# Optimization experiments

Hardware: AMD Instinct MI355X
Metric: run time of the kernel (lower is better)

## Reference

```python
import jax, jax.numpy as jnp
import numpy as np

A = 15                    # num_anchor_per_point
H = W = 34                # hardcoded feature map size in the torch module
STRIDE = 16               # heat_map_a
ANCHOR_W = jnp.array([45.3, 32.0, 22.6, 90.5, 64.0, 45.3, 181.0, 128.0, 90.5, 271.5, 192.0, 135.8, 362.0, 256.0, 181.0], dtype=jnp.float32)
ANCHOR_H = jnp.array([22.6, 32.0, 45.3, 45.3, 64.0, 90.5, 90.5, 128.0, 181.0, 135.8, 192.0, 271.5, 181.0, 256.0, 362.0], dtype=jnp.float32)
THRESH_OBJ = 0.2
MIN_H = 6.0
MIN_W = 6.0
MAX_CAND = 5000
TOP_N = 300
OVERLAP = 0.7


def _generate_anchors():
    xmins = -0.5 * (ANCHOR_W - 1.0)
    xmaxs = 0.5 * (ANCHOR_W - 1.0)
    ymins = -0.5 * (ANCHOR_H - 1.0)
    ymaxs = 0.5 * (ANCHOR_H - 1.0)
    return jnp.stack([xmins, ymins, xmaxs, ymaxs], axis=1)  # [A,4]


def _bbox_transform_inv(boxes, deltas):
    widths = boxes[:, 2] - boxes[:, 0] + 1.0
    heights = boxes[:, 3] - boxes[:, 1] + 1.0
    ctr_x = boxes[:, 0] + 0.5 * (widths - 1.0)
    ctr_y = boxes[:, 1] + 0.5 * (heights - 1.0)
    pred_ctr_x = deltas[:, 0] * widths + ctr_x
    pred_ctr_y = deltas[:, 1] * heights + ctr_y
    pred_w = jnp.exp(deltas[:, 2]) * widths
    pred_h = jnp.exp(deltas[:, 3]) * heights
    return jnp.stack([
        pred_ctr_x - 0.5 * (pred_w - 1.0),
        pred_ctr_y - 0.5 * (pred_h - 1.0),
        pred_ctr_x + 0.5 * (pred_w - 1.0),
        pred_ctr_y + 0.5 * (pred_h - 1.0),
    ], axis=1)


def _nms_keep(boxes, valid, thresh):
    # greedy NMS on score-descending boxes; +1 pixel convention matches module
    x1, y1, x2, y2 = boxes[:, 0], boxes[:, 1], boxes[:, 2], boxes[:, 3]
    areas = (x2 - x1 + 1.0) * (y2 - y1 + 1.0)
    iw = jnp.clip(jnp.minimum(x2[:, None], x2[None, :]) - jnp.maximum(x1[:, None], x1[None, :]) + 1.0, 0.0)
    ih = jnp.clip(jnp.minimum(y2[:, None], y2[None, :]) - jnp.maximum(y1[:, None], y1[None, :]) + 1.0, 0.0)
    inter = iw * ih
    iou = inter / (areas[:, None] + areas[None, :] - inter)  # [M,M]
    M = boxes.shape[0]
    idx = jnp.arange(M)

    def body(i, suppressed):
        alive = jnp.logical_not(suppressed[i])
        return suppressed | (alive & (iou[i] > thresh) & (idx > i))

    suppressed = jax.lax.fori_loop(0, M, body, jnp.logical_not(valid))
    return jnp.logical_not(suppressed) & valid


def _forward(rpn_cls_prob_reshape, rpn_bbox_pred, im_info, bbox_mean, bbox_std):
    origin_height = im_info[0].astype(jnp.float32)
    origin_width = im_info[1].astype(jnp.float32)

    # shifts (replicates torch meshgrid indexing='ij' and (y,x,y,x) column order)
    shift_x = jnp.arange(W, dtype=jnp.float32) * STRIDE
    shift_y = jnp.arange(H, dtype=jnp.float32) * STRIDE
    sx, sy = jnp.meshgrid(shift_x, shift_y, indexing='ij')  # [W,H]
    shifts = jnp.stack([sy.ravel(), sx.ravel(), sy.ravel(), sx.ravel()], axis=1)  # [W*H,4]
    anchors = (_generate_anchors()[None, :, :] + shifts[:, None, :]).reshape(-1, 4)  # [W*H*A,4]

    # deltas: [1,4A,34,34] -> (A,4,34,34) -> (34,34,A,4) -> (-1,4)
    deltas = rpn_bbox_pred.reshape(A, 4, H, W).transpose(2, 3, 0, 1).reshape(-1, 4)
    deltas = deltas * bbox_std + bbox_mean
    proposals = _bbox_transform_inv(anchors, deltas)

    # clip to image (refine_out_of_map_bbox=True)
    xs = jnp.clip(proposals[:, 0::2], 0.0, origin_width - 1.0)
    ys = jnp.clip(proposals[:, 1::2], 0.0, origin_height - 1.0)
    proposals = jnp.stack([xs[:, 0], ys[:, 0], xs[:, 1], ys[:, 1]], axis=1)

    # scores: [1,2A,34,34] -> (2,A,HW) -> (HW,A,2) -> (-1,2)
    scores = rpn_cls_prob_reshape.reshape(2, A, -1).transpose(2, 1, 0).reshape(-1, 2)

    # filter (HEIGHT_AND_WIDTH) via masking (jit-friendly, same selected set)
    ws = proposals[:, 2] - proposals[:, 0] + 1.0
    hs = proposals[:, 3] - proposals[:, 1] + 1.0
    keep = (scores[:, 1] > THRESH_OBJ) & (ws >= MIN_W) & (hs >= MIN_H)

    masked_score = jnp.where(keep, scores[:, 1], -1.0)
    top_vals, top_idx = jax.lax.top_k(masked_score, MAX_CAND)  # sorted descending
    cand = proposals[top_idx]
    valid = keep[top_idx]

    kept = _nms_keep(cand, valid, OVERLAP)

    # emit first TOP_N kept boxes in score order, zero-padded, with batch-id col 0
    rank = jnp.cumsum(kept.astype(jnp.int32)) - 1
    dest = jnp.where(kept & (rank < TOP_N), rank, TOP_N)
    out = jnp.zeros((TOP_N + 1, 5), dtype=cand.dtype)
    out = out.at[dest, 1:].set(cand)
    return out[:TOP_N]


def setup_inputs() -> dict:
    key = jax.random.key(0)
    k1, k2 = jax.random.split(key)
    rpn_cls_prob_reshape = jax.random.uniform(k1, (1, 2 * A, H, W), dtype=jnp.float32)
    rpn_bbox_pred = jax.random.normal(k2, (1, 4 * A, H, W), dtype=jnp.float32)
    im_info = jnp.array([544, 544], dtype=jnp.int32)
    bbox_mean = jnp.array([0.0, 0.0, 0.0, 0.0], dtype=jnp.float32)
    bbox_std = jnp.array([0.1, 0.1, 0.2, 0.2], dtype=jnp.float32)
    return {"rpn_cls_prob_reshape": rpn_cls_prob_reshape, "rpn_bbox_pred": rpn_bbox_pred,
            "im_info": im_info, "bbox_mean": bbox_mean, "bbox_std": bbox_std}


def reference(rpn_cls_prob_reshape, rpn_bbox_pred, im_info, bbox_mean, bbox_std):
    return _forward(rpn_cls_prob_reshape, rpn_bbox_pred, im_info, bbox_mean, bbox_std)
```

## Files before the change

### kernel.cpp

```cpp
#include <hip/hip_runtime.h>

#define NA 15
#define GH 34
#define GW 34
#define SP (GH*GW)
#define NB (SP*NA)
#define MAXC 5000
#define TOPN 300
#define NW 80
#define THRESH_OBJ 0.2f
#define NMS_T 0.7f
#define SH 12
#define BLO 0x3E4CCu
#define NBUCK 5120

typedef unsigned long long u64;
typedef unsigned int u32;

__constant__ float c_aw[NA] = {45.3f,32.0f,22.6f,90.5f,64.0f,45.3f,181.0f,128.0f,90.5f,271.5f,192.0f,135.8f,362.0f,256.0f,181.0f};
__constant__ float c_ah[NA] = {22.6f,32.0f,45.3f,45.3f,64.0f,90.5f,90.5f,128.0f,181.0f,135.8f,192.0f,271.5f,181.0f,256.0f,362.0f};

__global__ __launch_bounds__(256) void k_decode(
    const float* __restrict__ cls, const float* __restrict__ pred,
    const int* __restrict__ iminfo, const float* __restrict__ mean,
    const float* __restrict__ stdv, float* __restrict__ boxes,
    u32* __restrict__ sbits, int* __restrict__ hist) {
#pragma clang fp contract(off)
  int r = blockIdx.x * 256 + threadIdx.x;
  if (r >= NB) return;
  int n = r % NA;
  int p = r / NA;
  int w = p % GW;
  int h = p / GW;

  float score = cls[(NA + n) * SP + p];

  float d0 = pred[(n*4+0)*SP + p] * stdv[0] + mean[0];
  float d1 = pred[(n*4+1)*SP + p] * stdv[1] + mean[1];
  float d2 = pred[(n*4+2)*SP + p] * stdv[2] + mean[2];
  float d3 = pred[(n*4+3)*SP + p] * stdv[3] + mean[3];

  float aw = c_aw[n], ah = c_ah[n];
  float sx = (float)(w * 16);
  float sy = (float)(h * 16);
  float xmin = -0.5f * (aw - 1.0f) + sx;
  float ymin = -0.5f * (ah - 1.0f) + sy;
  float xmax =  0.5f * (aw - 1.0f) + sx;
  float ymax =  0.5f * (ah - 1.0f) + sy;

  float widths  = xmax - xmin + 1.0f;
  float heights = ymax - ymin + 1.0f;
  float ctrx = xmin + 0.5f * (widths - 1.0f);
  float ctry = ymin + 0.5f * (heights - 1.0f);

  float pcx = d0 * widths + ctrx;
  float pcy = d1 * heights + ctry;
  float pw = expf(d2) * widths;
  float ph = expf(d3) * heights;

  float x1 = pcx - 0.5f * (pw - 1.0f);
  float y1 = pcy - 0.5f * (ph - 1.0f);
  float x2 = pcx + 0.5f * (pw - 1.0f);
  float y2 = pcy + 0.5f * (ph - 1.0f);

  float ow = (float)iminfo[1] - 1.0f;
  float oh = (float)iminfo[0] - 1.0f;
  x1 = fminf(fmaxf(x1, 0.0f), ow);
  x2 = fminf(fmaxf(x2, 0.0f), ow);
  y1 = fminf(fmaxf(y1, 0.0f), oh);
  y2 = fminf(fmaxf(y2, 0.0f), oh);

  float ws = x2 - x1 + 1.0f;
  float hs = y2 - y1 + 1.0f;
  bool keep = (score > THRESH_OBJ) && (ws >= 6.0f) && (hs >= 6.0f);

  boxes[r*4+0] = x1;
  boxes[r*4+1] = y1;
  boxes[r*4+2] = x2;
  boxes[r*4+3] = y2;

  u32 bits = keep ? __float_as_uint(score) : 0u;
  sbits[r] = bits;
  if (bits) {
    int b = min((int)((bits >> SH) - BLO), NBUCK - 1);
    atomicAdd(&hist[b], 1);
  }
}

__global__ __launch_bounds__(1024) void k_scan(const int* __restrict__ hist,
    int* __restrict__ base, int* __restrict__ cnt) {
  __shared__ int sh[NBUCK];
  __shared__ int ch[1024];
  int tid = threadIdx.x;
  for (int j = tid; j < NBUCK; j += 1024) sh[j] = hist[j];
  __syncthreads();
  int c0 = sh[tid*5+0], c1 = sh[tid*5+1], c2 = sh[tid*5+2], c3 = sh[tid*5+3], c4 = sh[tid*5+4];
  ch[tid] = c0 + c1 + c2 + c3 + c4;
  __syncthreads();
  for (int off = 1; off < 1024; off <<= 1) {
    int v = ch[tid];
    int u = (tid + off < 1024) ? ch[tid + off] : 0;
    __syncthreads();
    ch[tid] = v + u;
    __syncthreads();
  }
  int S = (tid + 1 < 1024) ? ch[tid + 1] : 0;
  int b4 = S;
  int b3 = b4 + c4;
  int b2 = b3 + c3;
  int b1 = b2 + c2;
  int b0 = b1 + c1;
  base[tid*5+0] = b0; base[tid*5+1] = b1; base[tid*5+2] = b2;
  base[tid*5+3] = b3; base[tid*5+4] = b4;
  if (tid == 0) *cnt = ch[0];
}

__global__ __launch_bounds__(256) void k_place(const u32* __restrict__ sbits,
    const int* __restrict__ base, int* __restrict__ fill, u64* __restrict__ blist) {
  int i = blockIdx.x * 256 + threadIdx.x;
  if (i >= NB) return;
  u32 bits = sbits[i];
  if (!bits) return;
  int b = min((int)((bits >> SH) - BLO), NBUCK - 1);
  int pos = base[b] + atomicAdd(&fill[b], 1);
  blist[pos] = ((u64)bits << 32) | (u64)(0xFFFFFFFFu - (u32)i);
}

__global__ __launch_bounds__(256) void k_final(const u32* __restrict__ sbits,
    const int* __restrict__ hist, const int* __restrict__ base,
    const u64* __restrict__ blist, const float* __restrict__ boxes,
    float* __restrict__ sboxes) {
  int i = blockIdx.x * 256 + threadIdx.x;
  if (i >= NB) return;
  u32 bits = sbits[i];
  if (!bits) return;
  int b = min((int)((bits >> SH) - BLO), NBUCK - 1);
  u64 key = ((u64)bits << 32) | (u64)(0xFFFFFFFFu - (u32)i);
  int s = base[b], n = hist[b];
  int r = s;
  for (int p = s; p < s + n; ++p) r += (blist[p] > key) ? 1 : 0;
  if (r < MAXC) ((float4*)sboxes)[r] = ((const float4*)boxes)[i];
}

__global__ __launch_bounds__(64) void k_iou(const float* __restrict__ sboxes,
    const int* __restrict__ cnt, u64* __restrict__ mask) {
#pragma clang fp contract(off)
  int N = min(*cnt, MAXC);
  int bi = blockIdx.x, bj = blockIdx.y;
  int t = threadIdx.x;
  int i = bi * 64 + t;
  if (bj < bi) {
    if (i < N) mask[(size_t)i * NW + bj] = 0ULL;
    return;
  }
  if (bi * 64 >= N) return;
  __shared__ float4 jb[64];
  int j0 = bj * 64;
  if (j0 + t < N) jb[t] = ((const float4*)sboxes)[j0 + t];
  __syncthreads();
  if (i >= N) return;
  float4 a = ((const float4*)sboxes)[i];
  float areaA = (a.z - a.x + 1.0f) * (a.w - a.y + 1.0f);
  u64 word = 0;
  int jmax = min(64, N - j0);
  for (int jj = 0; jj < jmax; ++jj) {
    int j = j0 + jj;
    if (j <= i) continue;
    float4 b = jb[jj];
    float iw = fminf(a.z, b.z) - fmaxf(a.x, b.x) + 1.0f;
    float ih = fminf(a.w, b.w) - fmaxf(a.y, b.y) + 1.0f;
    iw = fmaxf(iw, 0.0f);
    ih = fmaxf(ih, 0.0f);
    float inter = iw * ih;
    float areaB = (b.z - b.x + 1.0f) * (b.w - b.y + 1.0f);
    float iou = inter / (areaA + areaB - inter);
    if (iou > NMS_T) word |= (1ULL << jj);
  }
  mask[(size_t)i * NW + bj] = word;
}

__device__ __forceinline__ u64 rl64(u64 v, int l) {
  unsigned lo = __builtin_amdgcn_readlane((unsigned)(v & 0xffffffffULL), l);
  unsigned hi = __builtin_amdgcn_readlane((unsigned)(v >> 32), l);
  return ((u64)hi << 32) | (u64)lo;
}

__global__ __launch_bounds__(64) void k_nms(const float* __restrict__ sboxes,
    const u64* __restrict__ mask, const int* __restrict__ cnt,
    float* __restrict__ out) {
  const int t = threadIdx.x;
  const int N = min(*cnt, MAXC);
  const int NBLK = (N + 63) >> 6;
  u64 r0 = 0ULL, r1 = 0ULL;
  __shared__ int klist[TOPN];
  int kept = 0;

  u64 colA = 0ULL, colB = 0ULL;
  if (NBLK > 0) colA = mask[(size_t)t * NW + 0];

  for (int b = 0; b < NBLK; ++b) {
    u64 cc = (b & 1) ? colB : colA;
    if (b + 1 < NBLK) {
      u64 nx = mask[(size_t)((b + 1) * 64 + t) * NW + (b + 1)];
      if (b & 1) colA = nx; else colB = nx;
    }
    int base = b * 64;
    int nv = N - base; if (nv > 64) nv = 64;
    u64 valid = (nv >= 64) ? ~0ULL : ((1ULL << nv) - 1ULL);
    u64 w = (b < 64) ? rl64(r0, b) : rl64(r1, b - 64);
    u64 avail = ~w & valid;
    u64 kmask = 0ULL;
    while (avail) {
      int d = __builtin_amdgcn_readfirstlane((int)__builtin_ctzll(avail));
      if (t == 0) klist[kept] = base + d;
      ++kept;
      kmask |= (1ULL << d);
      u64 sup = rl64(cc, d);
      avail &= ~(sup | (1ULL << d));
      if (kept >= TOPN) break;
    }
    if (kept >= TOPN) break;
    while (kmask) {
      u64 km = kmask;
      int n = __popcll(km); if (n > 8) n = 8;
#define NEXTD(dK) int dK = km ? (int)__builtin_ctzll(km) : 0; km &= (km - 1ULL);
      NEXTD(d0) NEXTD(d1) NEXTD(d2) NEXTD(d3) NEXTD(d4) NEXTD(d5) NEXTD(d6) NEXTD(d7)
#undef NEXTD
      kmask = km;
      u64 lo0=0,lo1=0,lo2=0,lo3=0,lo4=0,lo5=0,lo6=0,lo7=0;
      u64 hi0=0,hi1=0,hi2=0,hi3=0,hi4=0,hi5=0,hi6=0,hi7=0;
      int hw = 64 + (t & 15);
#define LOADK(K, dK) if (n > K) { const u64* rp = mask + (size_t)(base + dK) * NW; \
        lo##K = rp[t]; hi##K = rp[hw]; }
      LOADK(0, d0) LOADK(1, d1) LOADK(2, d2) LOADK(3, d3)
      LOADK(4, d4) LOADK(5, d5) LOADK(6, d6) LOADK(7, d7)
#undef LOADK
      r0 |= lo0 | lo1 | lo2 | lo3 | lo4 | lo5 | lo6 | lo7;
      r1 |= hi0 | hi1 | hi2 | hi3 | hi4 | hi5 | hi6 | hi7;
    }
  }
  __syncthreads();
  for (int e = t; e < TOPN * 5; e += 64) {
    int row = e / 5, col = e % 5;
    float v = 0.0f;
    if (col > 0 && row < kept) v = sboxes[klist[row] * 4 + (col - 1)];
    out[e] = v;
  }
}

extern "C" void kernel_launch(void* const* d_in, const int* in_sizes, int n_in,
                              void* d_out, int out_size, void* d_ws, size_t ws_size,
                              hipStream_t stream) {
  const float* cls  = (const float*)d_in[0];
  const float* pred = (const float*)d_in[1];
  const int*   imi  = (const int*)d_in[2];
  const float* mean = (const float*)d_in[3];
  const float* stdv = (const float*)d_in[4];
  float* out = (float*)d_out;

  char* ws = (char*)d_ws;
  float* boxes  = (float*)(ws);
  u32*   sbits  = (u32*)(ws + 277440);
  float* sboxes = (float*)(ws + 346800);
  int*   cnt    = (int*)(ws + 426800);
  int*   hist   = (int*)(ws + 426816);
  int*   fill   = (int*)(ws + 447296);
  int*   base   = (int*)(ws + 467776);
  u64*   mask   = (u64*)(ws + 488256);
  u64*   blist  = mask;

  hipMemsetAsync(hist, 0, 2 * NBUCK * sizeof(int), stream);

  k_decode<<<(NB + 255) / 256, 256, 0, stream>>>(cls, pred, imi, mean, stdv, boxes, sbits, hist);
  k_scan<<<1, 1024, 0, stream>>>(hist, base, cnt);
  k_place<<<(NB + 255) / 256, 256, 0, stream>>>(sbits, base, fill, blist);
  k_final<<<(NB + 255) / 256, 256, 0, stream>>>(sbits, hist, base, blist, boxes, sboxes);
  dim3 giou((MAXC + 63) / 64, NW);
  k_iou<<<giou, 64, 0, stream>>>(sboxes, cnt, mask);
  k_nms<<<1, 64, 0, stream>>>(sboxes, mask, cnt, out);
}
```

Measured before the change: 102.4 us.

## Fuse histogram/scan/place into one kernel and process NMS in 256-box steps

```diff
diff --git a/kernel.cpp b/kernel.cpp
--- a/kernel.cpp
+++ b/kernel.cpp
@@ -8,6 +8,7 @@
 #define MAXC 5000
 #define TOPN 300
 #define NW 80
+#define NRALLOC 5056
 #define THRESH_OBJ 0.2f
 #define NMS_T 0.7f
 #define SH 12
@@ -24,7 +25,7 @@
     const float* __restrict__ cls, const float* __restrict__ pred,
     const int* __restrict__ iminfo, const float* __restrict__ mean,
     const float* __restrict__ stdv, float* __restrict__ boxes,
-    u32* __restrict__ sbits, int* __restrict__ hist) {
+    u32* __restrict__ sbits) {
 #pragma clang fp contract(off)
   int r = blockIdx.x * 256 + threadIdx.x;
   if (r >= NB) return;
@@ -78,21 +79,21 @@
   boxes[r*4+1] = y1;
   boxes[r*4+2] = x2;
   boxes[r*4+3] = y2;
-
-  u32 bits = keep ? __float_as_uint(score) : 0u;
-  sbits[r] = bits;
-  if (bits) {
-    int b = min((int)((bits >> SH) - BLO), NBUCK - 1);
-    atomicAdd(&hist[b], 1);
-  }
-}
-
-__global__ __launch_bounds__(1024) void k_scan(const int* __restrict__ hist,
-    int* __restrict__ base, int* __restrict__ cnt) {
+  sbits[r] = keep ? __float_as_uint(score) : 0u;
+}
+
+__global__ __launch_bounds__(1024) void k_bucket(const u32* __restrict__ sbits,
+    int* __restrict__ base, int* __restrict__ cnt, u64* __restrict__ blist) {
   __shared__ int sh[NBUCK];
+  __shared__ int fl[NBUCK];
   __shared__ int ch[1024];
   int tid = threadIdx.x;
-  for (int j = tid; j < NBUCK; j += 1024) sh[j] = hist[j];
+  for (int j = tid; j < NBUCK; j += 1024) { sh[j] = 0; fl[j] = 0; }
+  __syncthreads();
+  for (int j = tid; j < NB; j += 1024) {
+    u32 bits = sbits[j];
+    if (bits) { int b = min((int)((bits >> SH) - BLO), NBUCK - 1); atomicAdd(&sh[b], 1); }
+  }
   __syncthreads();
   int c0 = sh[tid*5+0], c1 = sh[tid*5+1], c2 = sh[tid*5+2], c3 = sh[tid*5+3], c4 = sh[tid*5+4];
   ch[tid] = c0 + c1 + c2 + c3 + c4;
@@ -105,29 +106,28 @@
     __syncthreads();
   }
   int S = (tid + 1 < 1024) ? ch[tid + 1] : 0;
-  int b4 = S;
-  int b3 = b4 + c4;
-  int b2 = b3 + c3;
-  int b1 = b2 + c2;
-  int b0 = b1 + c1;
-  base[tid*5+0] = b0; base[tid*5+1] = b1; base[tid*5+2] = b2;
-  base[tid*5+3] = b3; base[tid*5+4] = b4;
+  int b4v = S;
+  int b3v = b4v + c4;
+  int b2v = b3v + c3;
+  int b1v = b2v + c2;
+  int b0v = b1v + c1;
+  base[tid*5+0] = b0v; base[tid*5+1] = b1v; base[tid*5+2] = b2v;
+  base[tid*5+3] = b3v; base[tid*5+4] = b4v;
+  sh[tid*5+0] = b0v; sh[tid*5+1] = b1v; sh[tid*5+2] = b2v;
+  sh[tid*5+3] = b3v; sh[tid*5+4] = b4v;
   if (tid == 0) *cnt = ch[0];
-}
-
-__global__ __launch_bounds__(256) void k_place(const u32* __restrict__ sbits,
-    const int* __restrict__ base, int* __restrict__ fill, u64* __restrict__ blist) {
-  int i = blockIdx.x * 256 + threadIdx.x;
-  if (i >= NB) return;
-  u32 bits = sbits[i];
-  if (!bits) return;
-  int b = min((int)((bits >> SH) - BLO), NBUCK - 1);
-  int pos = base[b] + atomicAdd(&fill[b], 1);
-  blist[pos] = ((u64)bits << 32) | (u64)(0xFFFFFFFFu - (u32)i);
+  __syncthreads();
+  for (int j = tid; j < NB; j += 1024) {
+    u32 bits = sbits[j];
+    if (!bits) continue;
+    int b = min((int)((bits >> SH) - BLO), NBUCK - 1);
+    int pos = sh[b] + atomicAdd(&fl[b], 1);
+    blist[pos] = ((u64)bits << 32) | (u64)(0xFFFFFFFFu - (u32)j);
+  }
 }
 
 __global__ __launch_bounds__(256) void k_final(const u32* __restrict__ sbits,
-    const int* __restrict__ hist, const int* __restrict__ base,
+    const int* __restrict__ base, const int* __restrict__ cnt,
     const u64* __restrict__ blist, const float* __restrict__ boxes,
     float* __restrict__ sboxes) {
   int i = blockIdx.x * 256 + threadIdx.x;
@@ -136,9 +136,10 @@
   if (!bits) return;
   int b = min((int)((bits >> SH) - BLO), NBUCK - 1);
   u64 key = ((u64)bits << 32) | (u64)(0xFFFFFFFFu - (u32)i);
-  int s = base[b], n = hist[b];
+  int s = base[b];
+  int e = (b > 0) ? base[b-1] : *cnt;
   int r = s;
-  for (int p = s; p < s + n; ++p) r += (blist[p] > key) ? 1 : 0;
+  for (int p = s; p < e; ++p) r += (blist[p] > key) ? 1 : 0;
   if (r < MAXC) ((float4*)sboxes)[r] = ((const float4*)boxes)[i];
 }
 
@@ -147,12 +148,9 @@
 #pragma clang fp contract(off)
   int N = min(*cnt, MAXC);
   int bi = blockIdx.x, bj = blockIdx.y;
+  if (bj < bi) return;
   int t = threadIdx.x;
   int i = bi * 64 + t;
-  if (bj < bi) {
-    if (i < N) mask[(size_t)i * NW + bj] = 0ULL;
-    return;
-  }
   if (bi * 64 >= N) return;
   __shared__ float4 jb[64];
   int j0 = bj * 64;
@@ -191,52 +189,72 @@
   const int t = threadIdx.x;
   const int N = min(*cnt, MAXC);
   const int NBLK = (N + 63) >> 6;
+  const int NSTEP = (NBLK + 3) >> 2;
+  const int hw = 64 + (t & 15);
   u64 r0 = 0ULL, r1 = 0ULL;
   __shared__ int klist[TOPN];
   int kept = 0;
 
-  u64 colA = 0ULL, colB = 0ULL;
-  if (NBLK > 0) colA = mask[(size_t)t * NW + 0];
-
-  for (int b = 0; b < NBLK; ++b) {
-    u64 cc = (b & 1) ? colB : colA;
-    if (b + 1 < NBLK) {
-      u64 nx = mask[(size_t)((b + 1) * 64 + t) * NW + (b + 1)];
-      if (b & 1) colA = nx; else colB = nx;
-    }
-    int base = b * 64;
-    int nv = N - base; if (nv > 64) nv = 64;
-    u64 valid = (nv >= 64) ? ~0ULL : ((1ULL << nv) - 1ULL);
-    u64 w = (b < 64) ? rl64(r0, b) : rl64(r1, b - 64);
-    u64 avail = ~w & valid;
-    u64 kmask = 0ULL;
-    while (avail) {
-      int d = __builtin_amdgcn_readfirstlane((int)__builtin_ctzll(avail));
-      if (t == 0) klist[kept] = base + d;
+  u64 cc00=0,cc01=0,cc02=0,cc03=0, cc11=0,cc12=0,cc13=0, cc22=0,cc23=0, cc33=0;
+#define CCL(g,k) { int rrow = sb + (g)*64 + t; rrow = (rrow < NRALLOC) ? rrow : 0; \
+    cc##g##k = mask[(size_t)rrow * NW + (wb + (k))]; }
+#define CC_ISSUE(S) { int sb = (S)*256, wb = (S)*4; \
+    CCL(0,0) CCL(0,1) CCL(0,2) CCL(0,3) \
+    CCL(1,1) CCL(1,2) CCL(1,3) \
+    CCL(2,2) CCL(2,3) \
+    CCL(3,3) }
+
+  if (NSTEP > 0) CC_ISSUE(0);
+
+  for (int s = 0; s < NSTEP; ++s) {
+    const int cbase = s * 256;
+    const int wb = s * 4;
+    u64 av0, av1, av2, av3;
+#define CARRY(K, dst) { int wi = wb + (K); \
+      u64 w = (wi < 64) ? rl64(r0, wi) : rl64(r1, wi - 64); \
+      int rem = N - wi * 64; \
+      u64 vm = (rem >= 64) ? ~0ULL : ((rem <= 0) ? 0ULL : ((1ULL << rem) - 1ULL)); \
+      dst = ~w & vm; }
+    CARRY(0, av0) CARRY(1, av1) CARRY(2, av2) CARRY(3, av3)
+#undef CARRY
+    int kept0 = kept;
+    for (;;) {
+      int d;
+      if (av0) d = (int)__builtin_ctzll(av0);
+      else if (av1) d = 64 + (int)__builtin_ctzll(av1);
+      else if (av2) d = 128 + (int)__builtin_ctzll(av2);
+      else if (av3) d = 192 + (int)__builtin_ctzll(av3);
+      else break;
+      d = __builtin_amdgcn_readfirstlane(d);
+      if (t == 0) klist[kept] = cbase + d;
       ++kept;
-      kmask |= (1ULL << d);
-      u64 sup = rl64(cc, d);
-      avail &= ~(sup | (1ULL << d));
       if (kept >= TOPN) break;
+      int l = d & 63;
+      u64 s0 = 0, s1 = 0, s2 = 0, s3 = 0;
+      switch (d >> 6) {
+        case 0: s0 = rl64(cc00, l) | (1ULL << l); s1 = rl64(cc01, l); s2 = rl64(cc02, l); s3 = rl64(cc03, l); break;
+        case 1: s1 = rl64(cc11, l) | (1ULL << l); s2 = rl64(cc12, l); s3 = rl64(cc13, l); break;
+        case 2: s2 = rl64(cc22, l) | (1ULL << l); s3 = rl64(cc23, l); break;
+        default: s3 = rl64(cc33, l) | (1ULL << l); break;
+      }
+      av0 &= ~s0; av1 &= ~s1; av2 &= ~s2; av3 &= ~s3;
     }
     if (kept >= TOPN) break;
-    while (kmask) {
-      u64 km = kmask;
-      int n = __popcll(km); if (n > 8) n = 8;
-#define NEXTD(dK) int dK = km ? (int)__builtin_ctzll(km) : 0; km &= (km - 1ULL);
-      NEXTD(d0) NEXTD(d1) NEXTD(d2) NEXTD(d3) NEXTD(d4) NEXTD(d5) NEXTD(d6) NEXTD(d7)
-#undef NEXTD
-      kmask = km;
-      u64 lo0=0,lo1=0,lo2=0,lo3=0,lo4=0,lo5=0,lo6=0,lo7=0;
-      u64 hi0=0,hi1=0,hi2=0,hi3=0,hi4=0,hi5=0,hi6=0,hi7=0;
-      int hw = 64 + (t & 15);
-#define LOADK(K, dK) if (n > K) { const u64* rp = mask + (size_t)(base + dK) * NW; \
-        lo##K = rp[t]; hi##K = rp[hw]; }
-      LOADK(0, d0) LOADK(1, d1) LOADK(2, d2) LOADK(3, d3)
-      LOADK(4, d4) LOADK(5, d5) LOADK(6, d6) LOADK(7, d7)
-#undef LOADK
-      r0 |= lo0 | lo1 | lo2 | lo3 | lo4 | lo5 | lo6 | lo7;
-      r1 |= hi0 | hi1 | hi2 | hi3 | hi4 | hi5 | hi6 | hi7;
+    if (s + 1 < NSTEP) CC_ISSUE(s + 1);
+    int nk = kept - kept0;
+    for (int c = 0; c < nk; c += 16) {
+      int m = nk - c;
+      u64 L0=0,L1=0,L2=0,L3=0,L4=0,L5=0,L6=0,L7=0,L8=0,L9=0,L10=0,L11=0,L12=0,L13=0,L14=0,L15=0;
+      u64 H0=0,H1=0,H2=0,H3=0,H4=0,H5=0,H6=0,H7=0,H8=0,H9=0,H10=0,H11=0,H12=0,H13=0,H14=0,H15=0;
+#define DRL(K) if (m > K) { int row = klist[kept0 + c + K]; int bk = row >> 6; \
+        const u64* rp = mask + (size_t)row * NW; \
+        u64 lv = rp[t]; u64 hv = rp[hw]; \
+        L##K = (t >= bk) ? lv : 0ULL; H##K = (hw >= bk) ? hv : 0ULL; }
+      DRL(0) DRL(1) DRL(2) DRL(3) DRL(4) DRL(5) DRL(6) DRL(7)
+      DRL(8) DRL(9) DRL(10) DRL(11) DRL(12) DRL(13) DRL(14) DRL(15)
+#undef DRL
+      r0 |= L0|L1|L2|L3|L4|L5|L6|L7|L8|L9|L10|L11|L12|L13|L14|L15;
+      r1 |= H0|H1|H2|H3|H4|H5|H6|H7|H8|H9|H10|H11|H12|H13|H14|H15;
     }
   }
   __syncthreads();
@@ -263,18 +281,13 @@
   u32*   sbits  = (u32*)(ws + 277440);
   float* sboxes = (float*)(ws + 346800);
   int*   cnt    = (int*)(ws + 426800);
-  int*   hist   = (int*)(ws + 426816);
-  int*   fill   = (int*)(ws + 447296);
-  int*   base   = (int*)(ws + 467776);
-  u64*   mask   = (u64*)(ws + 488256);
+  int*   base   = (int*)(ws + 426816);
+  u64*   mask   = (u64*)(ws + 447296);
   u64*   blist  = mask;
 
-  hipMemsetAsync(hist, 0, 2 * NBUCK * sizeof(int), stream);
-
-  k_decode<<<(NB + 255) / 256, 256, 0, stream>>>(cls, pred, imi, mean, stdv, boxes, sbits, hist);
-  k_scan<<<1, 1024, 0, stream>>>(hist, base, cnt);
-  k_place<<<(NB + 255) / 256, 256, 0, stream>>>(sbits, base, fill, blist);
-  k_final<<<(NB + 255) / 256, 256, 0, stream>>>(sbits, hist, base, blist, boxes, sboxes);
+  k_decode<<<(NB + 255) / 256, 256, 0, stream>>>(cls, pred, imi, mean, stdv, boxes, sbits);
+  k_bucket<<<1, 1024, 0, stream>>>(sbits, base, cnt, blist);
+  k_final<<<(NB + 255) / 256, 256, 0, stream>>>(sbits, base, cnt, blist, boxes, sboxes);
   dim3 giou((MAXC + 63) / 64, NW);
   k_iou<<<giou, 64, 0, stream>>>(sboxes, cnt, mask);
   k_nms<<<1, 64, 0, stream>>>(sboxes, mask, cnt, out);
```

After: 191.7 us. +87.2%, slower.

## Stream NMS suppression rows into LDS via async global_load_lds ring

Applied to the files above, without the earlier changes.

```diff
diff --git a/kernel.cpp b/kernel.cpp
--- a/kernel.cpp
+++ b/kernel.cpp
@@ -8,6 +8,7 @@
 #define MAXC 5000
 #define TOPN 300
 #define NW 80
+#define NRALLOC 5056
 #define THRESH_OBJ 0.2f
 #define NMS_T 0.7f
 #define SH 12
@@ -16,6 +17,7 @@
 
 typedef unsigned long long u64;
 typedef unsigned int u32;
+struct __align__(16) U2 { u64 x, y; };
 
 __constant__ float c_aw[NA] = {45.3f,32.0f,22.6f,90.5f,64.0f,45.3f,181.0f,128.0f,90.5f,271.5f,192.0f,135.8f,362.0f,256.0f,181.0f};
 __constant__ float c_ah[NA] = {22.6f,32.0f,45.3f,45.3f,64.0f,90.5f,90.5f,128.0f,181.0f,135.8f,192.0f,271.5f,181.0f,256.0f,362.0f};
@@ -78,7 +80,6 @@
   boxes[r*4+1] = y1;
   boxes[r*4+2] = x2;
   boxes[r*4+3] = y2;
-
   u32 bits = keep ? __float_as_uint(score) : 0u;
   sbits[r] = bits;
   if (bits) {
@@ -127,7 +128,7 @@
 }
 
 __global__ __launch_bounds__(256) void k_final(const u32* __restrict__ sbits,
-    const int* __restrict__ hist, const int* __restrict__ base,
+    const int* __restrict__ base, const int* __restrict__ cnt,
     const u64* __restrict__ blist, const float* __restrict__ boxes,
     float* __restrict__ sboxes) {
   int i = blockIdx.x * 256 + threadIdx.x;
@@ -136,9 +137,10 @@
   if (!bits) return;
   int b = min((int)((bits >> SH) - BLO), NBUCK - 1);
   u64 key = ((u64)bits << 32) | (u64)(0xFFFFFFFFu - (u32)i);
-  int s = base[b], n = hist[b];
+  int s = base[b];
+  int e = (b > 0) ? base[b-1] : *cnt;
   int r = s;
-  for (int p = s; p < s + n; ++p) r += (blist[p] > key) ? 1 : 0;
+  for (int p = s; p < e; ++p) r += (blist[p] > key) ? 1 : 0;
   if (r < MAXC) ((float4*)sboxes)[r] = ((const float4*)boxes)[i];
 }
 
@@ -185,59 +187,93 @@
   return ((u64)hi << 32) | (u64)lo;
 }
 
-__global__ __launch_bounds__(64) void k_nms(const float* __restrict__ sboxes,
+__device__ __forceinline__ void gload_lds16(const void* g, void* l) {
+  __builtin_amdgcn_global_load_lds(
+      (const __attribute__((address_space(1))) unsigned int*)g,
+      (__attribute__((address_space(3))) unsigned int*)l, 16, 0, 0);
+}
+
+__global__ __launch_bounds__(64, 1) void k_nms(const float* __restrict__ sboxes,
     const u64* __restrict__ mask, const int* __restrict__ cnt,
     float* __restrict__ out) {
   const int t = threadIdx.x;
   const int N = min(*cnt, MAXC);
   const int NBLK = (N + 63) >> 6;
-  u64 r0 = 0ULL, r1 = 0ULL;
-  __shared__ int klist[TOPN];
+  const int tt = (t < 40) ? t : 39;
+  const bool lane_ok = (t < 40);
+  u64 rv0 = 0ULL, rv1 = 0ULL;
+  __shared__ int klist[TOPN + 1];
+  __shared__ __align__(16) u64 ring[13 * 128];
   int kept = 0;
 
   u64 colA = 0ULL, colB = 0ULL;
   if (NBLK > 0) colA = mask[(size_t)t * NW + 0];
+  int pslot = 0;
+
+#define FLUSHRING(n_) do { \
+    asm volatile("s_waitcnt vmcnt(0)" ::: "memory"); \
+    __builtin_amdgcn_sched_barrier(0); \
+    int nf = (n_); \
+    U2 q0  = *(const U2*)(ring + 0*128  + 2*tt); \
+    U2 q1  = *(const U2*)(ring + 1*128  + 2*tt); \
+    U2 q2  = *(const U2*)(ring + 2*128  + 2*tt); \
+    U2 q3  = *(const U2*)(ring + 3*128  + 2*tt); \
+    U2 q4  = *(const U2*)(ring + 4*128  + 2*tt); \
+    U2 q5  = *(const U2*)(ring + 5*128  + 2*tt); \
+    U2 q6  = *(const U2*)(ring + 6*128  + 2*tt); \
+    U2 q7  = *(const U2*)(ring + 7*128  + 2*tt); \
+    U2 q8  = *(const U2*)(ring + 8*128  + 2*tt); \
+    U2 q9  = *(const U2*)(ring + 9*128  + 2*tt); \
+    U2 q10 = *(const U2*)(ring + 10*128 + 2*tt); \
+    U2 q11 = *(const U2*)(ring + 11*128 + 2*tt); \
+    u64 o0 = 0, o1 = 0; \
+    o0 |= (lane_ok && nf > 0)  ? q0.x  : 0ULL;  o1 |= (lane_ok && nf > 0)  ? q0.y  : 0ULL; \
+    o0 |= (lane_ok && nf > 1)  ? q1.x  : 0ULL;  o1 |= (lane_ok && nf > 1)  ? q1.y  : 0ULL; \
+    o0 |= (lane_ok && nf > 2)  ? q2.x  : 0ULL;  o1 |= (lane_ok && nf > 2)  ? q2.y  : 0ULL; \
+    o0 |= (lane_ok && nf > 3)  ? q3.x  : 0ULL;  o1 |= (lane_ok && nf > 3)  ? q3.y  : 0ULL; \
+    o0 |= (lane_ok && nf > 4)  ? q4.x  : 0ULL;  o1 |= (lane_ok && nf > 4)  ? q4.y  : 0ULL; \
+    o0 |= (lane_ok && nf > 5)  ? q5.x  : 0ULL;  o1 |= (lane_ok && nf > 5)  ? q5.y  : 0ULL; \
+    o0 |= (lane_ok && nf > 6)  ? q6.x  : 0ULL;  o1 |= (lane_ok && nf > 6)  ? q6.y  : 0ULL; \
+    o0 |= (lane_ok && nf > 7)  ? q7.x  : 0ULL;  o1 |= (lane_ok && nf > 7)  ? q7.y  : 0ULL; \
+    o0 |= (lane_ok && nf > 8)  ? q8.x  : 0ULL;  o1 |= (lane_ok && nf > 8)  ? q8.y  : 0ULL; \
+    o0 |= (lane_ok && nf > 9)  ? q9.x  : 0ULL;  o1 |= (lane_ok && nf > 9)  ? q9.y  : 0ULL; \
+    o0 |= (lane_ok && nf > 10) ? q10.x : 0ULL;  o1 |= (lane_ok && nf > 10) ? q10.y : 0ULL; \
+    o0 |= (lane_ok && nf > 11) ? q11.x : 0ULL;  o1 |= (lane_ok && nf > 11) ? q11.y : 0ULL; \
+    rv0 |= o0; rv1 |= o1; \
+  } while (0)
 
   for (int b = 0; b < NBLK; ++b) {
     u64 cc = (b & 1) ? colB : colA;
+    if (pslot > 0) { FLUSHRING(pslot); pslot = 0; }
+    int base = b * 64;
+    u64 w = rl64((b & 1) ? rv1 : rv0, b >> 1);
+    int nv = N - base; if (nv > 64) nv = 64;
+    u64 valid = (nv >= 64) ? ~0ULL : ((1ULL << nv) - 1ULL);
+    u64 avail = ~w & valid;
     if (b + 1 < NBLK) {
       u64 nx = mask[(size_t)((b + 1) * 64 + t) * NW + (b + 1)];
       if (b & 1) colA = nx; else colB = nx;
     }
-    int base = b * 64;
-    int nv = N - base; if (nv > 64) nv = 64;
-    u64 valid = (nv >= 64) ? ~0ULL : ((1ULL << nv) - 1ULL);
-    u64 w = (b < 64) ? rl64(r0, b) : rl64(r1, b - 64);
-    u64 avail = ~w & valid;
-    u64 kmask = 0ULL;
-    while (avail) {
-      int d = __builtin_amdgcn_readfirstlane((int)__builtin_ctzll(avail));
-      if (t == 0) klist[kept] = base + d;
-      ++kept;
-      kmask |= (1ULL << d);
-      u64 sup = rl64(cc, d);
-      avail &= ~(sup | (1ULL << d));
-      if (kept >= TOPN) break;
+    int slot = 0;
+    while (avail && kept < TOPN) {
+#pragma unroll
+      for (int u = 0; u < 4; ++u) {
+        bool on = (avail != 0ULL) && (kept < TOPN);
+        int d = (int)__builtin_ctzll(avail | (1ULL << 63));
+        int row = base + d;
+        klist[on ? kept : TOPN] = row;
+        gload_lds16((const char*)(mask + (size_t)row * NW) + (size_t)tt * 16,
+                    (void*)(ring + (size_t)(on ? slot : 12) * 128));
+        u64 sup = rl64(cc, d);
+        u64 clear = on ? (sup | (1ULL << d)) : 0ULL;
+        avail &= ~clear;
+        kept += on ? 1 : 0;
+        slot += on ? 1 : 0;
+      }
+      if (slot >= 8) { FLUSHRING(slot); slot = 0; }
     }
     if (kept >= TOPN) break;
-    while (kmask) {
-      u64 km = kmask;
-      int n = __popcll(km); if (n > 8) n = 8;
-#define NEXTD(dK) int dK = km ? (int)__builtin_ctzll(km) : 0; km &= (km - 1ULL);
-      NEXTD(d0) NEXTD(d1) NEXTD(d2) NEXTD(d3) NEXTD(d4) NEXTD(d5) NEXTD(d6) NEXTD(d7)
-#undef NEXTD
-      kmask = km;
-      u64 lo0=0,lo1=0,lo2=0,lo3=0,lo4=0,lo5=0,lo6=0,lo7=0;
-      u64 hi0=0,hi1=0,hi2=0,hi3=0,hi4=0,hi5=0,hi6=0,hi7=0;
-      int hw = 64 + (t & 15);
-#define LOADK(K, dK) if (n > K) { const u64* rp = mask + (size_t)(base + dK) * NW; \
-        lo##K = rp[t]; hi##K = rp[hw]; }
-      LOADK(0, d0) LOADK(1, d1) LOADK(2, d2) LOADK(3, d3)
-      LOADK(4, d4) LOADK(5, d5) LOADK(6, d6) LOADK(7, d7)
-#undef LOADK
-      r0 |= lo0 | lo1 | lo2 | lo3 | lo4 | lo5 | lo6 | lo7;
-      r1 |= hi0 | hi1 | hi2 | hi3 | hi4 | hi5 | hi6 | hi7;
-    }
+    pslot = slot;
   }
   __syncthreads();
   for (int e = t; e < TOPN * 5; e += 64) {
@@ -246,6 +282,7 @@
     if (col > 0 && row < kept) v = sboxes[klist[row] * 4 + (col - 1)];
     out[e] = v;
   }
+#undef FLUSHRING
 }
 
 extern "C" void kernel_launch(void* const* d_in, const int* in_sizes, int n_in,
@@ -274,7 +311,7 @@
   k_decode<<<(NB + 255) / 256, 256, 0, stream>>>(cls, pred, imi, mean, stdv, boxes, sbits, hist);
   k_scan<<<1, 1024, 0, stream>>>(hist, base, cnt);
   k_place<<<(NB + 255) / 256, 256, 0, stream>>>(sbits, base, fill, blist);
-  k_final<<<(NB + 255) / 256, 256, 0, stream>>>(sbits, hist, base, blist, boxes, sboxes);
+  k_final<<<(NB + 255) / 256, 256, 0, stream>>>(sbits, base, cnt, blist, boxes, sboxes);
   dim3 giou((MAXC + 63) / 64, NW);
   k_iou<<<giou, 64, 0, stream>>>(sboxes, cnt, mask);
   k_nms<<<1, 64, 0, stream>>>(sboxes, mask, cnt, out);
```

After: 96.61 us. 1.06x faster.
